# Performance work log

Measured on AMD Instinct MI355X. Metric: run time of the kernel, lower is better.

Reference implementation:

```python
import jax, jax.numpy as jnp
import numpy as np

D_MODEL = 1024
NUM_HEADS = 16
D_K = D_MODEL // NUM_HEADS


def setup_inputs() -> dict:
    key = jax.random.key(0)
    ks = jax.random.split(key, 11)
    B, S = 4, 2048
    s = 1.0 / np.sqrt(D_MODEL)
    return {
        "Q": jax.random.normal(ks[0], (B, S, D_MODEL), jnp.float32),
        "K": jax.random.normal(ks[1], (B, S, D_MODEL), jnp.float32),
        "V": jax.random.normal(ks[2], (B, S, D_MODEL), jnp.float32),
        "Wq": jax.random.normal(ks[3], (D_MODEL, D_MODEL), jnp.float32) * s,
        "bq": jax.random.normal(ks[4], (D_MODEL,), jnp.float32) * 0.01,
        "Wk": jax.random.normal(ks[5], (D_MODEL, D_MODEL), jnp.float32) * s,
        "bk": jax.random.normal(ks[6], (D_MODEL,), jnp.float32) * 0.01,
        "Wv": jax.random.normal(ks[7], (D_MODEL, D_MODEL), jnp.float32) * s,
        "bv": jax.random.normal(ks[8], (D_MODEL,), jnp.float32) * 0.01,
        "Wo": jax.random.normal(ks[9], (D_MODEL, D_MODEL), jnp.float32) * s,
        "bo": jax.random.normal(ks[10], (D_MODEL,), jnp.float32) * 0.01,
    }


def _split_heads(x):
    B, S, _ = x.shape
    return x.reshape(B, S, NUM_HEADS, D_K).transpose(0, 2, 1, 3)  # [B,H,S,Dk]


def reference(Q, K, V, Wq, bq, Wk, bk, Wv, bv, Wo, bo):
    # Linear layers (torch nn.Linear: x @ W.T + b)
    q = _split_heads(Q @ Wq.T + bq)
    k = _split_heads(K @ Wk.T + bk)
    v = _split_heads(V @ Wv.T + bv)
    scale = 1.0 / jnp.sqrt(jnp.asarray(D_K, jnp.float32))
    scores = jnp.einsum('bhqd,bhkd->bhqk', q, k) * scale  # [B,H,S,S]
    attn = jax.nn.softmax(scores, axis=-1)
    ctx = jnp.einsum('bhqk,bhkd->bhqd', attn, v)  # [B,H,S,Dk]
    B, H, S, Dk = ctx.shape
    ctx = ctx.transpose(0, 2, 1, 3).reshape(B, S, H * Dk)
    return ctx @ Wo.T + bo
```

## Files before the change

kernel.cpp:

```cpp
#include <hip/hip_runtime.h>
#include <hip/hip_bf16.h>

#define B_SZ 4
#define S_SZ 2048
#define D_SZ 1024
#define H_SZ 16
#define DK_SZ 64
#define M_ROWS (B_SZ * S_SZ)

typedef __bf16 bf16x8 __attribute__((ext_vector_type(8)));
typedef __bf16 bf16x4 __attribute__((ext_vector_type(4)));
typedef float  f32x4  __attribute__((ext_vector_type(4)));

typedef __attribute__((address_space(3))) unsigned int lds_u32;
typedef const __attribute__((address_space(1))) unsigned int glob_u32;

__device__ __forceinline__ bf16x8 load8(const float* p) {
    f32x4 a = *(const f32x4*)p;
    f32x4 b = *(const f32x4*)(p + 4);
    bf16x8 r;
    r[0] = (__bf16)a[0]; r[1] = (__bf16)a[1]; r[2] = (__bf16)a[2]; r[3] = (__bf16)a[3];
    r[4] = (__bf16)b[0]; r[5] = (__bf16)b[1]; r[6] = (__bf16)b[2]; r[7] = (__bf16)b[3];
    return r;
}
__device__ __forceinline__ bf16x8 load8(const __bf16* p) {
    return *(const bf16x8*)p;
}

__global__ __launch_bounds__(256)
void conv_bf16(const float* __restrict__ in, __bf16* __restrict__ out, int n8) {
    int i = blockIdx.x * 256 + threadIdx.x;
    const int stride = gridDim.x * 256;
    for (; i < n8; i += stride)
        *(bf16x8*)&out[(size_t)i * 8] = load8(in + (size_t)i * 8);
}

template <typename TC>
__global__ __launch_bounds__(256, 2)
void gemm_nt_bias_g(const __bf16* __restrict__ A, const __bf16* __restrict__ W,
                    const float* __restrict__ bias, TC* __restrict__ C,
                    int M, int N, int K) {
    __shared__ __align__(16) __bf16 sA[128 * 64];
    __shared__ __align__(16) __bf16 sB[128 * 64];
    const int tid = threadIdx.x;
    const int w = tid >> 6, lane = tid & 63;
    const int m0 = blockIdx.x * 128, n0 = blockIdx.y * 128;
    const int wr = w >> 1, wc = w & 1;
    const int lr = lane & 15, lq = lane >> 4;

    const int st_roff = lane >> 3;
    const int st_cg   = (lane & 7) ^ st_roff;

    f32x4 acc[4][4] = {};

    for (int kt = 0; kt < K; kt += 64) {
#pragma unroll
        for (int i = 0; i < 4; ++i) {
            const int seg = i * 4 + w;
            const int row = seg * 8 + st_roff;
            __builtin_amdgcn_global_load_lds(
                (glob_u32*)(A + (size_t)(m0 + row) * K + kt + st_cg * 8),
                (lds_u32*)(&sA[seg * 512]), 16, 0, 0);
            __builtin_amdgcn_global_load_lds(
                (glob_u32*)(W + (size_t)(n0 + row) * K + kt + st_cg * 8),
                (lds_u32*)(&sB[seg * 512]), 16, 0, 0);
        }
        __syncthreads();
#pragma unroll
        for (int s = 0; s < 2; ++s) {
            bf16x8 av[4], bv[4];
#pragma unroll
            for (int i = 0; i < 4; ++i)
                av[i] = *(const bf16x8*)&sA[(wr * 64 + i * 16 + lr) * 64
                                            + (((s * 4 + lq) ^ (lr & 7)) << 3)];
#pragma unroll
            for (int j = 0; j < 4; ++j)
                bv[j] = *(const bf16x8*)&sB[(wc * 64 + j * 16 + lr) * 64
                                            + (((s * 4 + lq) ^ (lr & 7)) << 3)];
#pragma unroll
            for (int i = 0; i < 4; ++i)
#pragma unroll
                for (int j = 0; j < 4; ++j)
                    acc[i][j] = __builtin_amdgcn_mfma_f32_16x16x32_bf16(
                        av[i], bv[j], acc[i][j], 0, 0, 0);
        }
        __syncthreads();
    }
#pragma unroll
    for (int j = 0; j < 4; ++j) {
        const int col = n0 + wc * 64 + j * 16 + lr;
        const float bias_f = bias[col];
#pragma unroll
        for (int i = 0; i < 4; ++i) {
            const int rbase = m0 + wr * 64 + i * 16 + lq * 4;
#pragma unroll
            for (int r = 0; r < 4; ++r)
                C[(size_t)(rbase + r) * N + col] = (TC)(acc[i][j][r] + bias_f);
        }
    }
}

#define SAST 72
template <typename TA, typename TW, typename TC>
__global__ __launch_bounds__(256, 2)
void gemm_nt_bias(const TA* __restrict__ A, const TW* __restrict__ W,
                  const float* __restrict__ bias, TC* __restrict__ C,
                  int M, int N, int K) {
    __shared__ __align__(16) __bf16 sA[128 * SAST];
    __shared__ __align__(16) __bf16 sB[128 * SAST];
    const int tid = threadIdx.x;
    const int w = tid >> 6, lane = tid & 63;
    const int m0 = blockIdx.x * 128, n0 = blockIdx.y * 128;
    const int wr = w >> 1, wc = w & 1;
    const int lr = lane & 15, lq = lane >> 4;

    f32x4 acc[4][4] = {};

    for (int kt = 0; kt < K; kt += 64) {
        for (int it = 0; it < 4; ++it) {
            const int c = it * 256 + tid;
            const int row = c >> 3, col8 = c & 7;
            *(bf16x8*)&sA[row * SAST + col8 * 8] =
                load8(A + (size_t)(m0 + row) * K + kt + col8 * 8);
            *(bf16x8*)&sB[row * SAST + col8 * 8] =
                load8(W + (size_t)(n0 + row) * K + kt + col8 * 8);
        }
        __syncthreads();
        for (int s = 0; s < 2; ++s) {
            bf16x8 av[4], bv[4];
            for (int i = 0; i < 4; ++i)
                av[i] = *(const bf16x8*)&sA[(wr * 64 + i * 16 + lr) * SAST + s * 32 + lq * 8];
            for (int j = 0; j < 4; ++j)
                bv[j] = *(const bf16x8*)&sB[(wc * 64 + j * 16 + lr) * SAST + s * 32 + lq * 8];
            for (int i = 0; i < 4; ++i)
                for (int j = 0; j < 4; ++j)
                    acc[i][j] = __builtin_amdgcn_mfma_f32_16x16x32_bf16(
                        av[i], bv[j], acc[i][j], 0, 0, 0);
        }
        __syncthreads();
    }
    for (int j = 0; j < 4; ++j) {
        const int col = n0 + wc * 64 + j * 16 + lr;
        const float bias_f = bias[col];
        for (int i = 0; i < 4; ++i) {
            const int rbase = m0 + wr * 64 + i * 16 + lq * 4;
            for (int r = 0; r < 4; ++r)
                C[(size_t)(rbase + r) * N + col] = (TC)(acc[i][j][r] + bias_f);
        }
    }
}

#define KVB 64
#define PST 72
__global__ __launch_bounds__(256, 2)
void attn_kernel(const __bf16* qm, const __bf16* __restrict__ km,
                 const __bf16* __restrict__ vm, __bf16* ctx) {
    __shared__ __align__(16) __bf16 sK[KVB * 64];
    __shared__ __align__(16) __bf16 sVt[64 * KVB];
    __shared__ __align__(16) __bf16 sP[8][16 * PST];

    const int tid = threadIdx.x, w = tid >> 6, lane = tid & 63;
    const int lr = lane & 15, lq = lane >> 4;
    const int bh = blockIdx.y, b = bh >> 4, h = bh & 15;
    const int q0 = blockIdx.x * 128;
    const size_t rowbase = (size_t)b * S_SZ;
    const int hoff = h * DK_SZ;

    bf16x8 qf[2][2];
#pragma unroll
    for (int qs = 0; qs < 2; ++qs) {
        const __bf16* qp = qm + (rowbase + q0 + w * 32 + qs * 16 + lr) * D_SZ + hoff;
        qf[qs][0] = *(const bf16x8*)(qp + lq * 8);
        qf[qs][1] = *(const bf16x8*)(qp + 32 + lq * 8);
    }

    float mrow[2] = {-1e30f, -1e30f};
    float lrow[2] = {0.f, 0.f};
    f32x4 o[2][4] = {};

    const int gl_koff = (lane >> 3);
    const int gl_c8 = lane & 7;
    const int v_key7 = tid >> 3, v_d8 = tid & 7;

    const __bf16* kbase = km + rowbase * D_SZ + hoff;
    const __bf16* vbase = vm + rowbase * D_SZ + hoff;

    for (int k0 = 0; k0 < S_SZ; k0 += KVB) {
#pragma unroll
        for (int i = 0; i < 2; ++i) {
            const int key = w * 16 + i * 8 + gl_koff;
            const __bf16* gp = kbase + (size_t)(k0 + key) * D_SZ
                               + ((gl_c8 ^ gl_koff) << 3);
            __builtin_amdgcn_global_load_lds(
                (glob_u32*)gp, (lds_u32*)(&sK[(w * 2 + i) * 512]), 16, 0, 0);
        }
#pragma unroll
        for (int p = 0; p < 2; ++p) {
            const int key = p * 32 + v_key7;
            bf16x8 vv = *(const bf16x8*)(vbase + (size_t)(k0 + key) * D_SZ + (v_d8 << 3));
            const int colbase = (((key >> 3) ^ v_d8) << 3) + (key & 7);
#pragma unroll
            for (int e = 0; e < 8; ++e)
                sVt[(v_d8 * 8 + e) * 64 + colbase] = vv[e];
        }
        __syncthreads();

        f32x4 sc[2][4] = {};
#pragma unroll
        for (int s = 0; s < 2; ++s) {
            bf16x8 kf[4];
#pragma unroll
            for (int nt = 0; nt < 4; ++nt)
                kf[nt] = *(const bf16x8*)&sK[(nt * 16 + lr) * 64
                                             + (((s * 4 + lq) ^ (lr & 7)) << 3)];
#pragma unroll
            for (int nt = 0; nt < 4; ++nt) {
                sc[0][nt] = __builtin_amdgcn_mfma_f32_16x16x32_bf16(
                    kf[nt], qf[0][s], sc[0][nt], 0, 0, 0);
                sc[1][nt] = __builtin_amdgcn_mfma_f32_16x16x32_bf16(
                    kf[nt], qf[1][s], sc[1][nt], 0, 0, 0);
            }
        }

#pragma unroll
        for (int qs = 0; qs < 2; ++qs) {
            float sv[4][4];
            float mt = -1e30f;
#pragma unroll
            for (int nt = 0; nt < 4; ++nt)
#pragma unroll
                for (int r = 0; r < 4; ++r) {
                    sv[nt][r] = sc[qs][nt][r] * 0.125f;
                    mt = fmaxf(mt, sv[nt][r]);
                }
            mt = fmaxf(mt, __shfl_xor(mt, 16));
            mt = fmaxf(mt, __shfl_xor(mt, 32));
            if (!__all(mt - mrow[qs] <= 8.f)) {
                const float mn = fmaxf(mrow[qs], mt);
                const float al = __expf(mrow[qs] - mn);
                mrow[qs] = mn;
                lrow[qs] *= al;
                float a4[4];
#pragma unroll
                for (int r = 0; r < 4; ++r)
                    a4[r] = __shfl(al, ((lane >> 4) << 2) + r, 64);
#pragma unroll
                for (int nt = 0; nt < 4; ++nt)
#pragma unroll
                    for (int r = 0; r < 4; ++r)
                        o[qs][nt][r] *= a4[r];
            }
            float ls = 0.f;
#pragma unroll
            for (int nt = 0; nt < 4; ++nt) {
                bf16x4 pk;
#pragma unroll
                for (int r = 0; r < 4; ++r) {
                    const float pv = __expf(sv[nt][r] - mrow[qs]);
                    ls += pv;
                    pk[r] = (__bf16)pv;
                }
                *(bf16x4*)&sP[w * 2 + qs][lr * PST + nt * 16 + lq * 4] = pk;
            }
            ls += __shfl_xor(ls, 16);
            ls += __shfl_xor(ls, 32);
            lrow[qs] += ls;
        }

        bf16x8 pf[2][2];
#pragma unroll
        for (int qs = 0; qs < 2; ++qs)
#pragma unroll
            for (int s = 0; s < 2; ++s)
                pf[qs][s] = *(const bf16x8*)&sP[w * 2 + qs][lr * PST + s * 32 + lq * 8];
#pragma unroll
        for (int s = 0; s < 2; ++s)
#pragma unroll
            for (int nt = 0; nt < 4; ++nt) {
                bf16x8 vf = *(const bf16x8*)&sVt[
                    (nt * 16 + lr) * 64
                    + (((s * 4 + lq) ^ (nt * 2 + (lr >> 3))) << 3)];
                o[0][nt] = __builtin_amdgcn_mfma_f32_16x16x32_bf16(
                    pf[0][s], vf, o[0][nt], 0, 0, 0);
                o[1][nt] = __builtin_amdgcn_mfma_f32_16x16x32_bf16(
                    pf[1][s], vf, o[1][nt], 0, 0, 0);
            }
        __syncthreads();
    }

#pragma unroll
    for (int qs = 0; qs < 2; ++qs) {
        const float linv = 1.f / lrow[qs];
        float l4[4];
#pragma unroll
        for (int r = 0; r < 4; ++r)
            l4[r] = __shfl(linv, ((lane >> 4) << 2) + r, 64);
#pragma unroll
        for (int nt = 0; nt < 4; ++nt) {
            const int col = hoff + nt * 16 + lr;
#pragma unroll
            for (int r = 0; r < 4; ++r) {
                const size_t row = rowbase + q0 + w * 32 + qs * 16 + lq * 4 + r;
                ctx[row * D_SZ + col] = (__bf16)(o[qs][nt][r] * l4[r]);
            }
        }
    }
}

extern "C" void kernel_launch(void* const* d_in, const int* in_sizes, int n_in,
                              void* d_out, int out_size, void* d_ws, size_t ws_size,
                              hipStream_t stream) {
    const float* Q  = (const float*)d_in[0];
    const float* K  = (const float*)d_in[1];
    const float* V  = (const float*)d_in[2];
    const float* Wq = (const float*)d_in[3];
    const float* bq = (const float*)d_in[4];
    const float* Wk = (const float*)d_in[5];
    const float* bk = (const float*)d_in[6];
    const float* Wv = (const float*)d_in[7];
    const float* bv = (const float*)d_in[8];
    const float* Wo = (const float*)d_in[9];
    const float* bo = (const float*)d_in[10];
    float* out = (float*)d_out;

    const size_t plane = (size_t)M_ROWS * D_SZ;
    const size_t wsz   = (size_t)D_SZ * D_SZ;
    const dim3 gg(M_ROWS / 128, D_SZ / 128), bb(256);
    const dim3 ag(S_SZ / 128, B_SZ * H_SZ);

    const size_t need_fast = (3 * plane + 4 * wsz) * sizeof(__bf16);
    if (ws_size >= need_fast) {
        __bf16* s0  = (__bf16*)d_ws;
        __bf16* qw  = s0 + plane;
        __bf16* kw  = s0 + 2 * plane;
        __bf16* wgt = s0 + 3 * plane;
        __bf16* vw  = (__bf16*)d_out;
        const int p8 = (int)(plane / 8), w8 = (int)(wsz / 8);

        conv_bf16<<<512, bb, 0, stream>>>(Wq, wgt, w8);
        conv_bf16<<<512, bb, 0, stream>>>(Wk, wgt + wsz, w8);
        conv_bf16<<<512, bb, 0, stream>>>(Wv, wgt + 2 * wsz, w8);
        conv_bf16<<<512, bb, 0, stream>>>(Wo, wgt + 3 * wsz, w8);

        conv_bf16<<<2048, bb, 0, stream>>>(Q, s0, p8);
        gemm_nt_bias_g<__bf16><<<gg, bb, 0, stream>>>(
            s0, wgt, bq, qw, M_ROWS, D_SZ, D_SZ);
        conv_bf16<<<2048, bb, 0, stream>>>(K, s0, p8);
        gemm_nt_bias_g<__bf16><<<gg, bb, 0, stream>>>(
            s0, wgt + wsz, bk, kw, M_ROWS, D_SZ, D_SZ);
        conv_bf16<<<2048, bb, 0, stream>>>(V, s0, p8);
        gemm_nt_bias_g<__bf16><<<gg, bb, 0, stream>>>(
            s0, wgt + 2 * wsz, bv, vw, M_ROWS, D_SZ, D_SZ);

        attn_kernel<<<ag, bb, 0, stream>>>(qw, kw, vw, qw);

        gemm_nt_bias_g<float><<<gg, bb, 0, stream>>>(
            qw, wgt + 3 * wsz, bo, out, M_ROWS, D_SZ, D_SZ);
        return;
    }

    if (ws_size < 2 * plane * sizeof(__bf16)) return;
    __bf16* qw = (__bf16*)d_ws;
    __bf16* kw = qw + plane;
    __bf16* vw = (__bf16*)d_out;
    __bf16* cw = qw;

    gemm_nt_bias<float, float, __bf16><<<gg, bb, 0, stream>>>(Q, Wq, bq, qw, M_ROWS, D_SZ, D_SZ);
    gemm_nt_bias<float, float, __bf16><<<gg, bb, 0, stream>>>(K, Wk, bk, kw, M_ROWS, D_SZ, D_SZ);
    gemm_nt_bias<float, float, __bf16><<<gg, bb, 0, stream>>>(V, Wv, bv, vw, M_ROWS, D_SZ, D_SZ);

    attn_kernel<<<ag, bb, 0, stream>>>(qw, kw, vw, cw);

    gemm_nt_bias<__bf16, float, float><<<gg, bb, 0, stream>>>(cw, Wo, bo, out,
                                                              M_ROWS, D_SZ, D_SZ);
}
```

Baseline: 395.2 us.

## Double-buffer LDS tiles in projection GEMM and remap blocks per XCD

Splits the LDS staging into two buffers so the next K-tile's global-to-LDS loads are issued before computing on the current tile, removing one barrier per iteration and overlapping memory with MFMA work. It also remaps block indices for the 64x8 grid so each XCD handles a contiguous band of M tiles, improving L2 reuse of A rows. LDS use doubles to 64KB per block, which may limit the two-blocks-per-CU occupancy.

Result: no change. 393.7 us (-0.4%).

```diff
diff --git a/kernel.cpp b/kernel.cpp
--- a/kernel.cpp
+++ b/kernel.cpp
@@ -40,11 +40,20 @@
 void gemm_nt_bias_g(const __bf16* __restrict__ A, const __bf16* __restrict__ W,
                     const float* __restrict__ bias, TC* __restrict__ C,
                     int M, int N, int K) {
-    __shared__ __align__(16) __bf16 sA[128 * 64];
-    __shared__ __align__(16) __bf16 sB[128 * 64];
+    __shared__ __align__(16) __bf16 sA[2][128 * 64];
+    __shared__ __align__(16) __bf16 sB[2][128 * 64];
     const int tid = threadIdx.x;
     const int w = tid >> 6, lane = tid & 63;
-    const int m0 = blockIdx.x * 128, n0 = blockIdx.y * 128;
+
+    int mt, nt;
+    if (gridDim.x == 64 && gridDim.y == 8) {
+        const int lin = blockIdx.x + blockIdx.y * 64;
+        const int xcd = lin & 7, idx = lin >> 3;
+        mt = xcd * 8 + (idx >> 3);
+        nt = idx & 7;
+    } else { mt = blockIdx.x; nt = blockIdx.y; }
+    const int m0 = mt * 128, n0 = nt * 128;
+
     const int wr = w >> 1, wc = w & 1;
     const int lr = lane & 15, lq = lane >> 4;
 
@@ -53,30 +62,31 @@
 
     f32x4 acc[4][4] = {};
 
-    for (int kt = 0; kt < K; kt += 64) {
+    auto STAGE = [&](int kt, int bsel) {
 #pragma unroll
         for (int i = 0; i < 4; ++i) {
             const int seg = i * 4 + w;
             const int row = seg * 8 + st_roff;
             __builtin_amdgcn_global_load_lds(
                 (glob_u32*)(A + (size_t)(m0 + row) * K + kt + st_cg * 8),
-                (lds_u32*)(&sA[seg * 512]), 16, 0, 0);
+                (lds_u32*)(&sA[bsel][seg * 512]), 16, 0, 0);
             __builtin_amdgcn_global_load_lds(
                 (glob_u32*)(W + (size_t)(n0 + row) * K + kt + st_cg * 8),
-                (lds_u32*)(&sB[seg * 512]), 16, 0, 0);
-        }
-        __syncthreads();
+                (lds_u32*)(&sB[bsel][seg * 512]), 16, 0, 0);
+        }
+    };
+    auto COMPUTE = [&](int bsel) {
 #pragma unroll
         for (int s = 0; s < 2; ++s) {
             bf16x8 av[4], bv[4];
 #pragma unroll
             for (int i = 0; i < 4; ++i)
-                av[i] = *(const bf16x8*)&sA[(wr * 64 + i * 16 + lr) * 64
-                                            + (((s * 4 + lq) ^ (lr & 7)) << 3)];
+                av[i] = *(const bf16x8*)&sA[bsel][(wr * 64 + i * 16 + lr) * 64
+                                                  + (((s * 4 + lq) ^ (lr & 7)) << 3)];
 #pragma unroll
             for (int j = 0; j < 4; ++j)
-                bv[j] = *(const bf16x8*)&sB[(wc * 64 + j * 16 + lr) * 64
-                                            + (((s * 4 + lq) ^ (lr & 7)) << 3)];
+                bv[j] = *(const bf16x8*)&sB[bsel][(wc * 64 + j * 16 + lr) * 64
+                                                  + (((s * 4 + lq) ^ (lr & 7)) << 3)];
 #pragma unroll
             for (int i = 0; i < 4; ++i)
 #pragma unroll
@@ -84,8 +94,19 @@
                     acc[i][j] = __builtin_amdgcn_mfma_f32_16x16x32_bf16(
                         av[i], bv[j], acc[i][j], 0, 0, 0);
         }
-        __syncthreads();
-    }
+    };
+
+    STAGE(0, 0);
+    __syncthreads();
+    int buf = 0;
+    for (int kt = 64; kt < K; kt += 64) {
+        STAGE(kt, buf ^ 1);
+        COMPUTE(buf);
+        __syncthreads();
+        buf ^= 1;
+    }
+    COMPUTE(buf);
+
 #pragma unroll
     for (int j = 0; j < 4; ++j) {
         const int col = n0 + wc * 64 + j * 16 + lr;
```
